# Performance work log

Hardware: AMD Instinct MI355X
Metric: run time of the kernel (lower is better)

Reference implementation:

```python
import jax, jax.numpy as jnp
import numpy as np

DIM, H, DH = 3072, 24, 128
MLP = int(DIM * 4.0)
EPS = 1e-6


def setup_inputs() -> dict:
    key = jax.random.key(0)
    ks = jax.random.split(key, 8)
    B, L = 2, 4096
    s = 0.02
    return {
        "hidden_states": jax.random.normal(ks[0], (B, L, DIM), jnp.float32),
        "temb": jax.random.normal(ks[1], (B, DIM), jnp.float32),
        "rope": jax.random.normal(ks[2], (L, DH // 2, 4), jnp.float32),
        "w_lin": jax.random.normal(ks[3], (DIM, 3 * DIM), jnp.float32) * s,
        "b_lin": jnp.zeros((3 * DIM,), jnp.float32),
        "w1": jax.random.normal(ks[4], (DIM, 3 * DIM + MLP), jnp.float32) * s,
        "b1": jnp.zeros((3 * DIM + MLP,), jnp.float32),
        "w2": jax.random.normal(ks[5], (DIM + MLP, DIM), jnp.float32) * s,
        "b2": jnp.zeros((DIM,), jnp.float32),
        "q_scale": jnp.ones((DH,), jnp.float32),
        "k_scale": jnp.ones((DH,), jnp.float32),
    }


def _rms(x, scale):
    return x * jax.lax.rsqrt(jnp.mean(x * x, axis=-1, keepdims=True) + EPS) * scale


def _rope(x, fr):
    # x: [B,H,L,DH]; fr: [L, DH//2, 2, 2]
    B, Hn, L, D = x.shape
    x_ = x.reshape(B, Hn, L, D // 2, 1, 2)
    out = fr[..., 0] * x_[..., 0] + fr[..., 1] * x_[..., 1]  # [B,H,L,D//2,2]
    return out.reshape(B, Hn, L, D)


def reference(hidden_states, temb, rope, w_lin, b_lin, w1, b1, w2, b2, q_scale, k_scale):
    B, L, _ = hidden_states.shape
    residual = hidden_states
    # AdaLayerNormZeroSingle
    emb = jax.nn.silu(temb) @ w_lin + b_lin  # [B, 3*DIM]
    shift, scale, gate = jnp.split(emb[:, None, :], 3, axis=-1)
    mu = jnp.mean(hidden_states, axis=-1, keepdims=True)
    var = jnp.mean(jnp.square(hidden_states - mu), axis=-1, keepdims=True)
    x = (hidden_states - mu) * jax.lax.rsqrt(var + EPS)
    x = x * (1 + scale) + shift
    # fused QKV + MLP projection
    proj = x @ w1 + b1
    qkv, mlp = proj[..., : 3 * DIM], proj[..., 3 * DIM :]
    qkv = qkv.reshape(B, L, 3, H, DH).transpose(2, 0, 3, 1, 4)  # [3,B,H,L,DH]
    q, k, v = qkv[0], qkv[1], qkv[2]
    q = _rms(q, q_scale)
    k = _rms(k, k_scale)
    fr = rope.reshape(L, DH // 2, 2, 2)
    q = _rope(q, fr)
    k = _rope(k, fr)
    # heads are MERGED before attention (faithful to source)
    q = q.transpose(0, 2, 1, 3).reshape(B, L, H * DH)
    k = k.transpose(0, 2, 1, 3).reshape(B, L, H * DH)
    v = v.transpose(0, 2, 1, 3).reshape(B, L, H * DH)
    attn = jax.nn.softmax(jnp.einsum("bqd,bkd->bqk", q, k) * (DH ** -0.5), axis=-1)
    attn_out = jnp.einsum("bqk,bkd->bqd", attn, v)
    h = jnp.concatenate([attn_out, jax.nn.gelu(mlp)], axis=-1) @ w2 + b2
    return residual + gate * h
```

## Files before the change

### kernel.cpp

```cpp
#include <hip/hip_runtime.h>
#include <hip/hip_fp16.h>

typedef _Float16 half_t;
typedef __attribute__((ext_vector_type(8))) _Float16 f16x8;
typedef __attribute__((ext_vector_type(4))) float f32x4;

#define DIM   3072
#define NH    24
#define DH    128
#define MLP_D 12288
#define LSEQ  4096
#define BATCH 2
#define NROWS 8192
#define N1    21504
#define QKV_N 9216
#define CAT_N 15360

__device__ __forceinline__ void gload16(const void* g, void* l) {
  __builtin_amdgcn_global_load_lds((const __attribute__((address_space(1))) void*)g,
                                   (__attribute__((address_space(3))) void*)l, 16, 0, 0);
}

__device__ __forceinline__ float gelu_tanh(float x) {
  float u = 0.7978845608028654f * (x + 0.044715f * x * x * x);
  float t = 1.f - 2.f / (__expf(2.f * u) + 1.f);
  return 0.5f * x * (1.f + t);
}

struct EpiParams {
  const float* bias;
  float* outF; int ldoF;
  half_t* o1; int ldo1;
  half_t* o2; int ldo2;
  const float* resid;
  const float* gate;
  float scale;
};

template<int EPI>
__global__ __launch_bounds__(512, 4) void gemm128(
    const half_t* __restrict__ A, int lda,
    const half_t* __restrict__ B, int ldb,
    int nbx, int nby, int nsplit, int K, EpiParams ep)
{
  __shared__ __align__(16) char lds[49152];
  const int t = threadIdx.x, lane = t & 63, wid = t >> 6;

  const int nwg = nbx * nby;
  const int wg = blockIdx.x;
  const int id = (wg & 7) * (nwg >> 3) + (wg >> 3);
  const int panel = 8 * nbx;
  const int bm = (id / panel) * 8 + (id % 8);
  const int bn = (id % panel) / 8;
  const int brow = bm * 128, bcol = bn * 256;
  const int wr = wid >> 2, wc = wid & 3;

  f32x4 acc[4][4];
#pragma unroll
  for (int m = 0; m < 4; ++m)
#pragma unroll
    for (int n = 0; n < 4; ++n) acc[m][n] = (f32x4){0.f, 0.f, 0.f, 0.f};

  const int scol = (((lane & 3) ^ ((lane >> 3) & 3)) * 8);
  const half_t* pA = A + (size_t)(brow + wid * 16 + (lane >> 2)) * lda + scol;
  const half_t* pB = B + (size_t)(bcol + wid * 32 + (lane >> 2)) * ldb + scol;
  const int NT = K >> 5;

  const int pc = (((lane >> 4) ^ ((lane >> 1) & 3)) << 4);
  const int arow  = (wr * 64 + (lane & 15)) * 64 + pc;
  const int brow_o = 8192 + (wc * 64 + (lane & 15)) * 64 + pc;

#define STAGE(tk) {                                                         \
    char* sb = lds + (((tk) & 1) ? 24576 : 0);                              \
    const half_t* ga = pA + (size_t)(tk) * 32;                              \
    const half_t* gb = pB + (size_t)(tk) * 32;                              \
    gload16(ga, sb + wid * 1024);                                           \
    gload16(gb, sb + 8192 + wid * 2048);                                    \
    gload16(gb + (size_t)16 * ldb, sb + 8192 + wid * 2048 + 1024); }

  STAGE(0)
  asm volatile("s_waitcnt vmcnt(0)" ::: "memory");
  __builtin_amdgcn_s_barrier();

  for (int tt = 0; tt < NT; ++tt) {
    char* cb = lds + ((tt & 1) ? 24576 : 0);
    if (tt + 1 < NT) STAGE(tt + 1)

    f16x8 af[4], bf[4];
#pragma unroll
    for (int mi = 0; mi < 4; ++mi) af[mi] = *(const f16x8*)(cb + arow + mi * 1024);
#pragma unroll
    for (int nj = 0; nj < 4; ++nj) bf[nj] = *(const f16x8*)(cb + brow_o + nj * 1024);
#pragma unroll
    for (int mi = 0; mi < 4; ++mi)
#pragma unroll
      for (int nj = 0; nj < 4; ++nj)
        acc[mi][nj] = __builtin_amdgcn_mfma_f32_16x16x32_f16(
            af[mi], bf[nj], acc[mi][nj], 0, 0, 0);

    __syncthreads();
  }
#undef STAGE

  const int laneR = lane & 15;
  const int colb = bcol + wc * 64;
  const int rowb = brow + wr * 64 + (lane >> 4) * 4;
#pragma unroll
  for (int mi = 0; mi < 4; ++mi) {
#pragma unroll
    for (int nj = 0; nj < 4; ++nj) {
      int col = colb + nj * 16 + laneR;
#pragma unroll
      for (int j = 0; j < 4; ++j) {
        int row = rowb + mi * 16 + j;
        float v = acc[mi][nj][j];
        if (EPI == 0) {
          v += ep.bias[col];
          if (col < nsplit) {
            ep.o1[(size_t)row * ep.ldo1 + col] = (half_t)v;
          } else {
            ep.o2[(size_t)row * ep.ldo2 + DIM + (col - nsplit)] = (half_t)gelu_tanh(v);
          }
        } else if (EPI == 1) {
          ep.outF[(size_t)row * ep.ldoF + col] = v * ep.scale;
        } else if (EPI == 2) {
          ep.o2[(size_t)row * ep.ldo2 + col] = (half_t)v;
        } else {
          v += ep.bias[col];
          int b = row >> 12;
          float g = ep.gate[(size_t)b * QKV_N + col];
          float r = ep.resid[(size_t)row * DIM + col];
          ep.outF[(size_t)row * ep.ldoF + col] = r + g * v;
        }
      }
    }
  }
}

__global__ __launch_bounds__(256) void k_emb(
    const float* __restrict__ temb, const float* __restrict__ w_lin,
    const float* __restrict__ b_lin, float* __restrict__ emb)
{
  __shared__ float s[DIM];
  int b = blockIdx.y;
  int col = blockIdx.x * 256 + threadIdx.x;
  const float* tr = temb + (size_t)b * DIM;
  for (int k = threadIdx.x; k < DIM; k += 256) {
    float x = tr[k];
    s[k] = x / (1.f + __expf(-x));
  }
  __syncthreads();
  float acc = b_lin[col];
  for (int k = 0; k < DIM; k += 4) {
    acc += s[k] * w_lin[(size_t)k * QKV_N + col]
         + s[k + 1] * w_lin[(size_t)(k + 1) * QKV_N + col]
         + s[k + 2] * w_lin[(size_t)(k + 2) * QKV_N + col]
         + s[k + 3] * w_lin[(size_t)(k + 3) * QKV_N + col];
  }
  emb[(size_t)b * QKV_N + col] = acc;
}

__global__ __launch_bounds__(256) void k_lnmod(
    const float* __restrict__ hs, const float* __restrict__ emb,
    half_t* __restrict__ xmod)
{
  int row = blockIdx.x;
  int b = row >> 12;
  const float* x = hs + (size_t)row * DIM;
  int t = threadIdx.x;
  float s = 0.f, s2 = 0.f;
  float4 v[3];
#pragma unroll
  for (int i = 0; i < 3; ++i) {
    v[i] = ((const float4*)x)[t + 256 * i];
    s  += v[i].x + v[i].y + v[i].z + v[i].w;
    s2 += v[i].x * v[i].x + v[i].y * v[i].y + v[i].z * v[i].z + v[i].w * v[i].w;
  }
  for (int o = 32; o; o >>= 1) { s += __shfl_xor(s, o); s2 += __shfl_xor(s2, o); }
  __shared__ float rs[4], rs2[4];
  int lane = t & 63, w = t >> 6;
  if (lane == 0) { rs[w] = s; rs2[w] = s2; }
  __syncthreads();
  s = rs[0] + rs[1] + rs[2] + rs[3];
  s2 = rs2[0] + rs2[1] + rs2[2] + rs2[3];
  float mu = s * (1.f / DIM);
  float var = s2 * (1.f / DIM) - mu * mu;
  float rstd = rsqrtf(var + 1e-6f);
  const float* shift = emb + (size_t)b * QKV_N;
  const float* scale = shift + DIM;
#pragma unroll
  for (int i = 0; i < 3; ++i) {
    int g = t + 256 * i;
    float4 sc = ((const float4*)scale)[g];
    float4 sh = ((const float4*)shift)[g];
    half_t ob[4];
    float vv[4] = {v[i].x, v[i].y, v[i].z, v[i].w};
    float scv[4] = {sc.x, sc.y, sc.z, sc.w};
    float shv[4] = {sh.x, sh.y, sh.z, sh.w};
#pragma unroll
    for (int j = 0; j < 4; ++j) {
      float xn = (vv[j] - mu) * rstd;
      ob[j] = (half_t)(xn * (1.f + scv[j]) + shv[j]);
    }
    *(uint2*)&xmod[(size_t)row * DIM + g * 4] = *(uint2*)ob;
  }
}

__global__ __launch_bounds__(256) void k_transpose_cvt(
    const float* __restrict__ in, half_t* __restrict__ out, int R, int C)
{
  __shared__ float s[64][65];
  int c0 = blockIdx.x * 64, r0 = blockIdx.y * 64;
  int tx = threadIdx.x & 63, ty = threadIdx.x >> 6;
#pragma unroll
  for (int j = 0; j < 16; ++j) {
    int r = ty + j * 4;
    s[r][tx] = in[(size_t)(r0 + r) * C + c0 + tx];
  }
  __syncthreads();
#pragma unroll
  for (int j = 0; j < 16; ++j) {
    int c = ty + j * 4;
    out[(size_t)(c0 + c) * R + r0 + tx] = (half_t)s[tx][c];
  }
}

__global__ __launch_bounds__(256) void k_qk_rmsrope(
    half_t* __restrict__ qkv, const float* __restrict__ rope,
    const float* __restrict__ q_scale, const float* __restrict__ k_scale)
{
  int w = blockIdx.x * 4 + (threadIdx.x >> 6);
  int lane = threadIdx.x & 63;
  int qk = w & 1;
  int hr = w >> 1;
  int h = hr % 24;
  int bl = hr / 24;
  size_t base = (size_t)bl * QKV_N + qk * DIM + h * DH;
  float x0 = (float)qkv[base + lane * 2];
  float x1 = (float)qkv[base + lane * 2 + 1];
  float ss = x0 * x0 + x1 * x1;
  for (int o = 32; o; o >>= 1) ss += __shfl_xor(ss, o);
  float r = rsqrtf(ss * (1.f / DH) + 1e-6f);
  const float* sc = qk ? k_scale : q_scale;
  float xs0 = x0 * r * sc[lane * 2];
  float xs1 = x1 * r * sc[lane * 2 + 1];
  int l = bl & (LSEQ - 1);
  float4 fr = ((const float4*)rope)[(size_t)l * 64 + lane];
  qkv[base + lane * 2]     = (half_t)(fr.x * xs0 + fr.y * xs1);
  qkv[base + lane * 2 + 1] = (half_t)(fr.z * xs0 + fr.w * xs1);
}

__global__ __launch_bounds__(256) void k_vT(
    const half_t* __restrict__ qkv, half_t* __restrict__ vT)
{
  __shared__ half_t s[64][65];
  int b = blockIdx.z;
  int l0 = blockIdx.x * 64, d0 = blockIdx.y * 64;
  int tx = threadIdx.x & 63, ty = threadIdx.x >> 6;
#pragma unroll
  for (int j = 0; j < 16; ++j) {
    int l = ty + j * 4;
    s[l][tx] = qkv[(size_t)(b * LSEQ + l0 + l) * QKV_N + 2 * DIM + d0 + tx];
  }
  __syncthreads();
#pragma unroll
  for (int j = 0; j < 16; ++j) {
    int d = ty + j * 4;
    vT[((size_t)b * DIM + d0 + d) * LSEQ + l0 + tx] = s[tx][d];
  }
}

__global__ __launch_bounds__(256) void k_softmax(
    const float* __restrict__ S, half_t* __restrict__ P)
{
  int row = blockIdx.x;
  const float* srow = S + (size_t)row * LSEQ;
  int t = threadIdx.x;
  float4 v[4];
  float mx = -1e30f;
#pragma unroll
  for (int i = 0; i < 4; ++i) {
    v[i] = ((const float4*)srow)[t + 256 * i];
    mx = fmaxf(mx, fmaxf(fmaxf(v[i].x, v[i].y), fmaxf(v[i].z, v[i].w)));
  }
  for (int o = 32; o; o >>= 1) mx = fmaxf(mx, __shfl_xor(mx, o));
  __shared__ float rmx[4], rsum[4];
  int lane = t & 63, w = t >> 6;
  if (lane == 0) rmx[w] = mx;
  __syncthreads();
  mx = fmaxf(fmaxf(rmx[0], rmx[1]), fmaxf(rmx[2], rmx[3]));
  float s = 0.f;
#pragma unroll
  for (int i = 0; i < 4; ++i) {
    v[i].x = __expf(v[i].x - mx); v[i].y = __expf(v[i].y - mx);
    v[i].z = __expf(v[i].z - mx); v[i].w = __expf(v[i].w - mx);
    s += v[i].x + v[i].y + v[i].z + v[i].w;
  }
  for (int o = 32; o; o >>= 1) s += __shfl_xor(s, o);
  if (lane == 0) rsum[w] = s;
  __syncthreads();
  s = rsum[0] + rsum[1] + rsum[2] + rsum[3];
  float inv = 1.f / s;
#pragma unroll
  for (int i = 0; i < 4; ++i) {
    half_t ob[4] = {
      (half_t)(v[i].x * inv), (half_t)(v[i].y * inv),
      (half_t)(v[i].z * inv), (half_t)(v[i].w * inv)};
    *(uint2*)&P[(size_t)row * LSEQ + (t + 256 * i) * 4] = *(uint2*)ob;
  }
}

extern "C" void kernel_launch(void* const* d_in, const int* in_sizes, int n_in,
                              void* d_out, int out_size, void* d_ws, size_t ws_size,
                              hipStream_t stream) {
  const float* hs      = (const float*)d_in[0];
  const float* temb    = (const float*)d_in[1];
  const float* rope    = (const float*)d_in[2];
  const float* w_lin   = (const float*)d_in[3];
  const float* b_lin   = (const float*)d_in[4];
  const float* w1      = (const float*)d_in[5];
  const float* b1      = (const float*)d_in[6];
  const float* w2      = (const float*)d_in[7];
  const float* b2      = (const float*)d_in[8];
  const float* q_scale = (const float*)d_in[9];
  const float* k_scale = (const float*)d_in[10];
  float* out = (float*)d_out;

  char* ws = (char*)d_ws;
  size_t off = 0;
  auto alloc = [&](size_t bytes) { char* p = ws + off; off += (bytes + 255) & ~(size_t)255; return p; };
  float*  emb    = (float*) alloc((size_t)BATCH * QKV_N * 4);
  half_t* xmod   = (half_t*)alloc((size_t)NROWS * DIM * 2);
  half_t* w1T    = (half_t*)alloc((size_t)N1 * DIM * 2);
  half_t* w2T    = (half_t*)alloc((size_t)DIM * CAT_N * 2);
  half_t* qkv    = (half_t*)alloc((size_t)NROWS * QKV_N * 2);
  half_t* concat = (half_t*)alloc((size_t)NROWS * CAT_N * 2);
  half_t* vT     = (half_t*)alloc((size_t)BATCH * DIM * LSEQ * 2);
  float*  Sbuf   = (float*) alloc((size_t)LSEQ * LSEQ * 4);
  half_t* Pbuf   = (half_t*)alloc((size_t)LSEQ * LSEQ * 2);
  (void)ws_size; (void)n_in; (void)in_sizes; (void)out_size;

  k_emb<<<dim3(QKV_N / 256, BATCH), 256, 0, stream>>>(temb, w_lin, b_lin, emb);
  k_transpose_cvt<<<dim3(N1 / 64, DIM / 64), 256, 0, stream>>>(w1, w1T, DIM, N1);
  k_transpose_cvt<<<dim3(DIM / 64, CAT_N / 64), 256, 0, stream>>>(w2, w2T, CAT_N, DIM);
  k_lnmod<<<NROWS, 256, 0, stream>>>(hs, emb, xmod);

  EpiParams ep1 = {b1, nullptr, 0, qkv, QKV_N, concat, CAT_N, nullptr, nullptr, 0.f};
  gemm128<0><<<(N1 / 256) * (NROWS / 128), 512, 0, stream>>>(
      xmod, DIM, w1T, DIM, N1 / 256, NROWS / 128, QKV_N, DIM, ep1);

  k_qk_rmsrope<<<(NROWS * NH * 2) / 4, 256, 0, stream>>>(qkv, rope, q_scale, k_scale);
  k_vT<<<dim3(LSEQ / 64, DIM / 64, BATCH), 256, 0, stream>>>(qkv, vT);

  for (int b = 0; b < BATCH; ++b) {
    const half_t* qb = qkv + (size_t)b * LSEQ * QKV_N;
    EpiParams epS = {nullptr, Sbuf, LSEQ, nullptr, 0, nullptr, 0, nullptr, nullptr, 0.08838834764831845f};
    gemm128<1><<<(LSEQ / 256) * (LSEQ / 128), 512, 0, stream>>>(
        qb, QKV_N, qb + DIM, QKV_N, LSEQ / 256, LSEQ / 128, 0, DIM, epS);
    k_softmax<<<LSEQ, 256, 0, stream>>>(Sbuf, Pbuf);
    EpiParams epPV = {nullptr, nullptr, 0, nullptr, 0,
                      concat + (size_t)b * LSEQ * CAT_N, CAT_N, nullptr, nullptr, 0.f};
    gemm128<2><<<(DIM / 256) * (LSEQ / 128), 512, 0, stream>>>(
        Pbuf, LSEQ, vT + (size_t)b * DIM * LSEQ, LSEQ, DIM / 256, LSEQ / 128, 0, LSEQ, epPV);
  }

  EpiParams ep2 = {b2, out, DIM, nullptr, 0, nullptr, 0, hs, emb + 2 * DIM, 0.f};
  gemm128<3><<<(DIM / 256) * (NROWS / 128), 512, 0, stream>>>(
      concat, CAT_N, w2T, CAT_N, DIM / 256, NROWS / 128, 0, CAT_N, ep2);
}
```

Measured before the change: 3.016 ms.

## Triple-buffer GEMM LDS pipeline with register prefetch and store attention scores in fp16

The GEMM main loop moves from double to triple-buffered LDS staging. Fragments for the next tile are read into registers after a single barrier per iteration, and MFMA issue priority is raised with setprio, so that global loads, LDS reads and MFMAs overlap better. LDS use grows from 48KB to 72KB, which may lower occupancy against the declared launch bounds. Separately, the attention score matrix is now written and read as fp16 instead of fp32, halving its memory traffic in the softmax path, at the risk of losing precision or overflowing on large logits.

```diff
diff --git a/kernel.cpp b/kernel.cpp
--- a/kernel.cpp
+++ b/kernel.cpp
@@ -43,7 +43,7 @@
     const half_t* __restrict__ B, int ldb,
     int nbx, int nby, int nsplit, int K, EpiParams ep)
 {
-  __shared__ __align__(16) char lds[49152];
+  __shared__ __align__(16) char lds[73728];
   const int t = threadIdx.x, lane = t & 63, wid = t >> 6;
 
   const int nwg = nbx * nby;
@@ -70,37 +70,57 @@
   const int arow  = (wr * 64 + (lane & 15)) * 64 + pc;
   const int brow_o = 8192 + (wc * 64 + (lane & 15)) * 64 + pc;
 
-#define STAGE(tk) {                                                         \
-    char* sb = lds + (((tk) & 1) ? 24576 : 0);                              \
+  f16x8 af[4], bf[4];
+
+#define STAGE(tk, slot) {                                                   \
+    char* sb = lds + (slot) * 24576;                                        \
     const half_t* ga = pA + (size_t)(tk) * 32;                              \
     const half_t* gb = pB + (size_t)(tk) * 32;                              \
     gload16(ga, sb + wid * 1024);                                           \
     gload16(gb, sb + 8192 + wid * 2048);                                    \
     gload16(gb + (size_t)16 * ldb, sb + 8192 + wid * 2048 + 1024); }
 
-  STAGE(0)
-  asm volatile("s_waitcnt vmcnt(0)" ::: "memory");
+#define READF(slot) {                                                       \
+    char* cb = lds + (slot) * 24576;                                        \
+    af[0] = *(const f16x8*)(cb + arow);                                     \
+    af[1] = *(const f16x8*)(cb + arow + 1024);                              \
+    af[2] = *(const f16x8*)(cb + arow + 2048);                              \
+    af[3] = *(const f16x8*)(cb + arow + 3072);                              \
+    bf[0] = *(const f16x8*)(cb + brow_o);                                   \
+    bf[1] = *(const f16x8*)(cb + brow_o + 1024);                            \
+    bf[2] = *(const f16x8*)(cb + brow_o + 2048);                            \
+    bf[3] = *(const f16x8*)(cb + brow_o + 3072); }
+
+  STAGE(0, 0) STAGE(1, 1)
+  asm volatile("s_waitcnt vmcnt(3)" ::: "memory");
   __builtin_amdgcn_s_barrier();
-
+  __builtin_amdgcn_sched_barrier(0);
+  READF(0)
+
+  int s0 = 0, s1 = 1, s2 = 2;
   for (int tt = 0; tt < NT; ++tt) {
-    char* cb = lds + ((tt & 1) ? 24576 : 0);
-    if (tt + 1 < NT) STAGE(tt + 1)
-
-    f16x8 af[4], bf[4];
-#pragma unroll
-    for (int mi = 0; mi < 4; ++mi) af[mi] = *(const f16x8*)(cb + arow + mi * 1024);
-#pragma unroll
-    for (int nj = 0; nj < 4; ++nj) bf[nj] = *(const f16x8*)(cb + brow_o + nj * 1024);
+    __builtin_amdgcn_s_setprio(1);
 #pragma unroll
     for (int mi = 0; mi < 4; ++mi)
 #pragma unroll
       for (int nj = 0; nj < 4; ++nj)
         acc[mi][nj] = __builtin_amdgcn_mfma_f32_16x16x32_f16(
             af[mi], bf[nj], acc[mi][nj], 0, 0, 0);
-
-    __syncthreads();
+    __builtin_amdgcn_s_setprio(0);
+
+    if (tt + 2 < NT) STAGE(tt + 2, s2)
+
+    if (tt + 2 < NT)      asm volatile("s_waitcnt vmcnt(3)" ::: "memory");
+    else if (tt + 1 < NT) asm volatile("s_waitcnt vmcnt(0)" ::: "memory");
+    __builtin_amdgcn_s_barrier();
+    __builtin_amdgcn_sched_barrier(0);
+
+    if (tt + 1 < NT) READF(s1)
+
+    int tmp = s0; s0 = s1; s1 = s2; s2 = tmp;
   }
 #undef STAGE
+#undef READF
 
   const int laneR = lane & 15;
   const int colb = bcol + wc * 64;
@@ -122,7 +142,7 @@
             ep.o2[(size_t)row * ep.ldo2 + DIM + (col - nsplit)] = (half_t)gelu_tanh(v);
           }
         } else if (EPI == 1) {
-          ep.outF[(size_t)row * ep.ldoF + col] = v * ep.scale;
+          ep.o1[(size_t)row * ep.ldo1 + col] = (half_t)(v * ep.scale);
         } else if (EPI == 2) {
           ep.o2[(size_t)row * ep.ldo2 + col] = (half_t)v;
         } else {
@@ -271,17 +291,22 @@
 }
 
 __global__ __launch_bounds__(256) void k_softmax(
-    const float* __restrict__ S, half_t* __restrict__ P)
+    const half_t* __restrict__ S, half_t* __restrict__ P)
 {
   int row = blockIdx.x;
-  const float* srow = S + (size_t)row * LSEQ;
+  const half_t* srow = S + (size_t)row * LSEQ;
   int t = threadIdx.x;
-  float4 v[4];
+  f16x8 hv[2];
+  float vf[16];
   float mx = -1e30f;
 #pragma unroll
-  for (int i = 0; i < 4; ++i) {
-    v[i] = ((const float4*)srow)[t + 256 * i];
-    mx = fmaxf(mx, fmaxf(fmaxf(v[i].x, v[i].y), fmaxf(v[i].z, v[i].w)));
+  for (int i = 0; i < 2; ++i) {
+    hv[i] = ((const f16x8*)srow)[t + 256 * i];
+#pragma unroll
+    for (int j = 0; j < 8; ++j) {
+      vf[i * 8 + j] = (float)hv[i][j];
+      mx = fmaxf(mx, vf[i * 8 + j]);
+    }
   }
   for (int o = 32; o; o >>= 1) mx = fmaxf(mx, __shfl_xor(mx, o));
   __shared__ float rmx[4], rsum[4];
@@ -291,10 +316,9 @@
   mx = fmaxf(fmaxf(rmx[0], rmx[1]), fmaxf(rmx[2], rmx[3]));
   float s = 0.f;
 #pragma unroll
-  for (int i = 0; i < 4; ++i) {
-    v[i].x = __expf(v[i].x - mx); v[i].y = __expf(v[i].y - mx);
-    v[i].z = __expf(v[i].z - mx); v[i].w = __expf(v[i].w - mx);
-    s += v[i].x + v[i].y + v[i].z + v[i].w;
+  for (int i = 0; i < 16; ++i) {
+    vf[i] = __expf(vf[i] - mx);
+    s += vf[i];
   }
   for (int o = 32; o; o >>= 1) s += __shfl_xor(s, o);
   if (lane == 0) rsum[w] = s;
@@ -302,11 +326,11 @@
   s = rsum[0] + rsum[1] + rsum[2] + rsum[3];
   float inv = 1.f / s;
 #pragma unroll
-  for (int i = 0; i < 4; ++i) {
-    half_t ob[4] = {
-      (half_t)(v[i].x * inv), (half_t)(v[i].y * inv),
-      (half_t)(v[i].z * inv), (half_t)(v[i].w * inv)};
-    *(uint2*)&P[(size_t)row * LSEQ + (t + 256 * i) * 4] = *(uint2*)ob;
+  for (int i = 0; i < 2; ++i) {
+    f16x8 ob;
+#pragma unroll
+    for (int j = 0; j < 8; ++j) ob[j] = (half_t)(vf[i * 8 + j] * inv);
+    ((f16x8*)&P[(size_t)row * LSEQ])[t + 256 * i] = ob;
   }
 }
 
@@ -336,7 +360,7 @@
   half_t* qkv    = (half_t*)alloc((size_t)NROWS * QKV_N * 2);
   half_t* concat = (half_t*)alloc((size_t)NROWS * CAT_N * 2);
   half_t* vT     = (half_t*)alloc((size_t)BATCH * DIM * LSEQ * 2);
-  float*  Sbuf   = (float*) alloc((size_t)LSEQ * LSEQ * 4);
+  half_t* Sbuf   = (half_t*)alloc((size_t)LSEQ * LSEQ * 2);
   half_t* Pbuf   = (half_t*)alloc((size_t)LSEQ * LSEQ * 2);
   (void)ws_size; (void)n_in; (void)in_sizes; (void)out_size;
 
@@ -354,7 +378,7 @@
 
   for (int b = 0; b < BATCH; ++b) {
     const half_t* qb = qkv + (size_t)b * LSEQ * QKV_N;
-    EpiParams epS = {nullptr, Sbuf, LSEQ, nullptr, 0, nullptr, 0, nullptr, nullptr, 0.08838834764831845f};
+    EpiParams epS = {nullptr, nullptr, 0, Sbuf, LSEQ, nullptr, 0, nullptr, nullptr, 0.08838834764831845f};
     gemm128<1><<<(LSEQ / 256) * (LSEQ / 128), 512, 0, stream>>>(
         qb, QKV_N, qb + DIM, QKV_N, LSEQ / 256, LSEQ / 128, 0, DIM, epS);
     k_softmax<<<LSEQ, 256, 0, stream>>>(Sbuf, Pbuf);
```

Result: faster. 2.823 ms (-6.4%).
